# Kernel optimization log

Measured on AMD Instinct MI355X. Metric: run time of the kernel, lower is better.

Reference implementation:

```python
import jax, jax.numpy as jnp
import numpy as np

N, E = 50000, 800000
IN_DIM, HIDDEN, OUT_DIM, LAYERS = 128, 64, 40, 3


def setup_inputs() -> dict:
    key = jax.random.key(0)
    ks = jax.random.split(key, 12)
    glorot = lambda k, fi, fo: jax.random.normal(k, (fi, fo), jnp.float32) * np.sqrt(2.0 / (fi + fo)).astype(np.float32)
    return {
        "x": jax.random.normal(ks[0], (N, IN_DIM), jnp.float32),
        "edge_index": jax.random.randint(ks[1], (2, E), 0, N, jnp.int64),
        "edge_weight": jax.random.uniform(ks[2], (E,), jnp.float32),
        "W1": glorot(ks[3], IN_DIM, HIDDEN), "b1": jnp.zeros((HIDDEN,), jnp.float32),
        "W2": glorot(ks[4], HIDDEN, HIDDEN), "b2": jnp.zeros((HIDDEN,), jnp.float32),
        "W3": glorot(ks[5], HIDDEN, HIDDEN), "b3": jnp.zeros((HIDDEN,), jnp.float32),
        "Wlin": glorot(ks[6], HIDDEN * LAYERS, OUT_DIM), "blin": jnp.zeros((OUT_DIM,), jnp.float32),
    }


def reference(x, edge_index, edge_weight, W1, b1, W2, b2, W3, b3, Wlin, blin):
    src, dst = edge_index[0], edge_index[1]

    def gcn_conv(h, W, b):
        # GCNConv with normalize=False: linear transform, then weighted sum aggregation at dst, then bias.
        h = h @ W                                   # [N, hidden]
        msg = h[src] * edge_weight[:, None]          # [E, hidden] gather + scale
        agg = jax.ops.segment_sum(msg, dst, num_segments=h.shape[0])  # scatter-add
        return agg + b

    outs = []
    h = x
    for W, b in ((W1, b1), (W2, b2), (W3, b3)):
        h = jax.nn.relu(gcn_conv(h, W, b))           # dropout is identity at inference
        outs.append(h)

    hjk = jnp.concatenate(outs, axis=-1)             # JumpingKnowledge mode='cat' -> [N, hidden*layers]
    return hjk @ Wlin + blin                         # [N, out_dim]
```

## Files before the change

### kernel.cpp

```cpp
#include <hip/hip_runtime.h>

#define HID 64
#define JK_DIM 192
#define OUT_DIM 40
#define AP 136
#define HP 72

typedef __attribute__((ext_vector_type(8))) short bf16x8;
typedef __attribute__((ext_vector_type(4))) float f32x4;

__device__ inline unsigned short f2b(float f) {
    unsigned u = __float_as_uint(f);
    unsigned r = u + 0x7FFF + ((u >> 16) & 1);
    return (unsigned short)(r >> 16);
}
__device__ inline float b2f(unsigned short u) {
    return __uint_as_float(((unsigned)u) << 16);
}
__device__ inline float blo(unsigned u) { return __uint_as_float(u << 16); }
__device__ inline float bhi(unsigned u) { return __uint_as_float(u & 0xFFFF0000u); }
__device__ inline unsigned pack2(float a, float b) {
    return (unsigned)f2b(a) | ((unsigned)f2b(b) << 16);
}

__global__ __launch_bounds__(256) void prep(int* __restrict__ deg, int n,
                                            int* __restrict__ gctr,
                                            const float* __restrict__ W1,
                                            const float* __restrict__ W2,
                                            const float* __restrict__ W3,
                                            const float* __restrict__ Wlin,
                                            unsigned short* __restrict__ W1T,
                                            unsigned short* __restrict__ W2T,
                                            unsigned short* __restrict__ W3T,
                                            unsigned short* __restrict__ WlinT) {
    int i = blockIdx.x * 256 + threadIdx.x;
    if (i == 0) gctr[0] = 0;
    if (i < n) deg[i] = 0;
    if (i < 64 * 128) {
        int nn = i >> 7, k = i & 127;
        W1T[i] = f2b(W1[k * 64 + nn]);
    }
    if (i < 64 * 64) {
        int nn = i >> 6, k = i & 63;
        W2T[i] = f2b(W2[k * 64 + nn]);
        W3T[i] = f2b(W3[k * 64 + nn]);
    }
    if (i < 48 * JK_DIM) {
        int c = i / JK_DIM, k = i - c * JK_DIM;
        WlinT[i] = (c < OUT_DIM) ? f2b(Wlin[k * OUT_DIM + c]) : (unsigned short)0;
    }
}

__global__ __launch_bounds__(256) void hist_dst(const int* __restrict__ dst,
                                                int* __restrict__ deg,
                                                unsigned short* __restrict__ rank,
                                                int E, int part) {
    int p = blockIdx.x & 7;
    int bid = blockIdx.x >> 3;
    int nblk = gridDim.x >> 3;
    int lo = p * part, hi = lo + part;
    int E4 = E >> 2;
    for (int q = bid * 256 + threadIdx.x; q < E4; q += nblk * 256) {
        int4 d4 = ((const int4*)dst)[q];
        int e = q * 4;
        if (d4.x >= lo && d4.x < hi) rank[e + 0] = (unsigned short)atomicAdd(&deg[d4.x], 1);
        if (d4.y >= lo && d4.y < hi) rank[e + 1] = (unsigned short)atomicAdd(&deg[d4.y], 1);
        if (d4.z >= lo && d4.z < hi) rank[e + 2] = (unsigned short)atomicAdd(&deg[d4.z], 1);
        if (d4.w >= lo && d4.w < hi) rank[e + 3] = (unsigned short)atomicAdd(&deg[d4.w], 1);
    }
    if (bid == 0 && threadIdx.x < (E & 3)) {
        int e = (E & ~3) + threadIdx.x;
        int d = dst[e];
        if (d >= lo && d < hi) rank[e] = (unsigned short)atomicAdd(&deg[d], 1);
    }
}

__global__ __launch_bounds__(256) void scan_fused(const int* __restrict__ deg,
                                                  int* __restrict__ off,
                                                  int* __restrict__ gctr, int n) {
    __shared__ int tmp[256];
    __shared__ int base;
    int i = blockIdx.x * 256 + threadIdx.x;
    int v = (i < n) ? deg[i] : 0;
    tmp[threadIdx.x] = v;
    __syncthreads();
    for (int d = 1; d < 256; d <<= 1) {
        int t = (threadIdx.x >= d) ? tmp[threadIdx.x - d] : 0;
        __syncthreads();
        tmp[threadIdx.x] += t;
        __syncthreads();
    }
    if (threadIdx.x == 255) base = atomicAdd(gctr, tmp[255]);
    __syncthreads();
    if (i < n) off[i] = base + tmp[threadIdx.x] - v;
}

__global__ __launch_bounds__(256) void fill_and_gemm(
        const int* __restrict__ src, const int* __restrict__ dst,
        const float* __restrict__ ew, const int* __restrict__ off,
        const unsigned short* __restrict__ rank,
        unsigned* __restrict__ ecsr, int E,
        const float* __restrict__ x, const unsigned short* __restrict__ W1T,
        unsigned short* __restrict__ linb, int n, int nFill) {
    __shared__ unsigned short Ah[64 * AP];
    __shared__ unsigned short Wt[64 * AP];
    int tid = threadIdx.x;
    if ((int)blockIdx.x < nFill) {
        int q = blockIdx.x * 256 + tid;
        int E4 = E >> 2;
        if (q < E4) {
            int4 d4 = ((const int4*)dst)[q];
            int4 s4 = ((const int4*)src)[q];
            float4 wv = ((const float4*)ew)[q];
            ushort4 r4 = ((const ushort4*)rank)[q];
            ecsr[off[d4.x] + r4.x] = (unsigned)s4.x | ((unsigned)f2b(wv.x) << 16);
            ecsr[off[d4.y] + r4.y] = (unsigned)s4.y | ((unsigned)f2b(wv.y) << 16);
            ecsr[off[d4.z] + r4.z] = (unsigned)s4.z | ((unsigned)f2b(wv.z) << 16);
            ecsr[off[d4.w] + r4.w] = (unsigned)s4.w | ((unsigned)f2b(wv.w) << 16);
        }
        if (blockIdx.x == 0 && tid < (E & 3)) {
            int e = (E & ~3) + tid;
            int d = dst[e];
            ecsr[off[d] + rank[e]] = (unsigned)src[e] | ((unsigned)f2b(ew[e]) << 16);
        }
        return;
    }
    int row0 = (blockIdx.x - nFill) * 64;
    if (row0 >= n) return;
    for (int i = tid; i < 64 * 32; i += 256) {
        int r = i >> 5;
        int c4 = (i & 31) * 4;
        int grow = row0 + r;
        if (grow >= n) grow = n - 1;
        float4 v = *(const float4*)(x + (long)grow * 128 + c4);
        ushort4 o;
        o.x = f2b(v.x); o.y = f2b(v.y); o.z = f2b(v.z); o.w = f2b(v.w);
        *(ushort4*)(Ah + r * AP + c4) = o;
    }
    for (int i = tid; i < 64 * 16; i += 256) {
        int nn = i >> 4;
        int k8 = (i & 15) * 8;
        *(uint4*)(Wt + nn * AP + k8) = *(const uint4*)(W1T + nn * 128 + k8);
    }
    __syncthreads();

    int wave = tid >> 6;
    int lane = tid & 63;
    int lr = lane & 15;
    int lk = (lane >> 4) * 8;
    f32x4 acc[4];
#pragma unroll
    for (int nf = 0; nf < 4; ++nf) acc[nf] = (f32x4){0.f, 0.f, 0.f, 0.f};
#pragma unroll
    for (int k0 = 0; k0 < 128; k0 += 32) {
        bf16x8 a = *(const bf16x8*)(Ah + (wave * 16 + lr) * AP + k0 + lk);
#pragma unroll
        for (int nf = 0; nf < 4; ++nf) {
            bf16x8 b = *(const bf16x8*)(Wt + (nf * 16 + lr) * AP + k0 + lk);
            acc[nf] = __builtin_amdgcn_mfma_f32_16x16x32_bf16(a, b, acc[nf], 0, 0, 0);
        }
    }
    int mbase = wave * 16 + (lane >> 4) * 4;
#pragma unroll
    for (int nf = 0; nf < 4; ++nf) {
#pragma unroll
        for (int r = 0; r < 4; ++r) {
            int grow = row0 + mbase + r;
            if (grow < n)
                linb[(long)grow * HID + nf * 16 + lr] = f2b(acc[nf][r]);
        }
    }
}

__global__ __launch_bounds__(256) void aggregate(const unsigned short* __restrict__ linb,
                                                 const unsigned* __restrict__ ecsr,
                                                 const int* __restrict__ off,
                                                 const int* __restrict__ deg,
                                                 const float* __restrict__ bias,
                                                 unsigned short* __restrict__ hout, int n) {
    int cl = threadIdx.x & 7;
    float4 bLo = *(const float4*)(bias + cl * 8);
    float4 bHi = *(const float4*)(bias + cl * 8 + 4);
    int grp = (blockIdx.x * 256 + threadIdx.x) >> 3;
    int ngrp = (gridDim.x * 256) >> 3;
    for (int node = grp; node < n; node += ngrp) {
        int start = off[node];
        int cnt = deg[node];
        float acc[8];
#pragma unroll
        for (int i = 0; i < 8; ++i) acc[i] = 0.f;

        int s[8];
        float w[8];
#pragma unroll
        for (int t = 0; t < 8; ++t) {
            s[t] = 0; w[t] = 0.f;
            if (t < cnt) {
                unsigned m = ecsr[start + t];
                s[t] = (int)(m & 0xFFFFu);
                w[t] = b2f((unsigned short)(m >> 16));
            }
        }
        for (int bb = 0; bb < cnt; bb += 8) {
            int s2[8];
            float w2[8];
#pragma unroll
            for (int t = 0; t < 8; ++t) {
                int e = bb + 8 + t;
                s2[t] = 0; w2[t] = 0.f;
                if (e < cnt) {
                    unsigned m = ecsr[start + e];
                    s2[t] = (int)(m & 0xFFFFu);
                    w2[t] = b2f((unsigned short)(m >> 16));
                }
            }
            uint4 u[8];
#pragma unroll
            for (int t = 0; t < 8; ++t)
                u[t] = *(const uint4*)(linb + (long)s[t] * HID + cl * 8);
#pragma unroll
            for (int t = 0; t < 8; ++t) {
                acc[0] += blo(u[t].x) * w[t];
                acc[1] += bhi(u[t].x) * w[t];
                acc[2] += blo(u[t].y) * w[t];
                acc[3] += bhi(u[t].y) * w[t];
                acc[4] += blo(u[t].z) * w[t];
                acc[5] += bhi(u[t].z) * w[t];
                acc[6] += blo(u[t].w) * w[t];
                acc[7] += bhi(u[t].w) * w[t];
            }
#pragma unroll
            for (int t = 0; t < 8; ++t) { s[t] = s2[t]; w[t] = w2[t]; }
        }

        uint4 o;
        o.x = pack2(fmaxf(acc[0] + bLo.x, 0.f), fmaxf(acc[1] + bLo.y, 0.f));
        o.y = pack2(fmaxf(acc[2] + bLo.z, 0.f), fmaxf(acc[3] + bLo.w, 0.f));
        o.z = pack2(fmaxf(acc[4] + bHi.x, 0.f), fmaxf(acc[5] + bHi.y, 0.f));
        o.w = pack2(fmaxf(acc[6] + bHi.z, 0.f), fmaxf(acc[7] + bHi.w, 0.f));
        *(uint4*)(hout + (long)node * JK_DIM + cl * 8) = o;
    }
}

__global__ __launch_bounds__(256) void agg_transform(
        const unsigned short* __restrict__ hprev,
        const unsigned* __restrict__ ecsr,
        const int* __restrict__ off, const int* __restrict__ deg,
        const unsigned short* __restrict__ WT, const float* __restrict__ bias,
        unsigned short* __restrict__ hout, int n) {
    __shared__ unsigned short Hs[64 * HP];
    __shared__ unsigned short Wt[64 * HP];
    int tid = threadIdx.x;
    int row0 = blockIdx.x * 64;
    if (row0 >= n) return;
    for (int i = tid; i < 64 * 8; i += 256) {
        int nn = i >> 3;
        int k8 = (i & 7) * 8;
        *(uint4*)(Wt + nn * HP + k8) = *(const uint4*)(WT + nn * 64 + k8);
    }
    int cl = tid & 7;
    int g0 = tid >> 3;
    for (int gi = 0; gi < 2; ++gi) {
        int lrow = g0 + gi * 32;
        int node = row0 + lrow;
        float acc[8];
#pragma unroll
        for (int i = 0; i < 8; ++i) acc[i] = 0.f;
        if (node < n) {
            int start = off[node];
            int cnt = deg[node];
            int s[8];
            float w[8];
#pragma unroll
            for (int t = 0; t < 8; ++t) {
                s[t] = 0; w[t] = 0.f;
                if (t < cnt) {
                    unsigned m = ecsr[start + t];
                    s[t] = (int)(m & 0xFFFFu);
                    w[t] = b2f((unsigned short)(m >> 16));
                }
            }
            for (int bb = 0; bb < cnt; bb += 8) {
                int s2[8];
                float w2[8];
#pragma unroll
                for (int t = 0; t < 8; ++t) {
                    int e = bb + 8 + t;
                    s2[t] = 0; w2[t] = 0.f;
                    if (e < cnt) {
                        unsigned m = ecsr[start + e];
                        s2[t] = (int)(m & 0xFFFFu);
                        w2[t] = b2f((unsigned short)(m >> 16));
                    }
                }
                uint4 u[8];
#pragma unroll
                for (int t = 0; t < 8; ++t)
                    u[t] = *(const uint4*)(hprev + (long)s[t] * JK_DIM + cl * 8);
#pragma unroll
                for (int t = 0; t < 8; ++t) {
                    acc[0] += blo(u[t].x) * w[t];
                    acc[1] += bhi(u[t].x) * w[t];
                    acc[2] += blo(u[t].y) * w[t];
                    acc[3] += bhi(u[t].y) * w[t];
                    acc[4] += blo(u[t].z) * w[t];
                    acc[5] += bhi(u[t].z) * w[t];
                    acc[6] += blo(u[t].w) * w[t];
                    acc[7] += bhi(u[t].w) * w[t];
                }
#pragma unroll
                for (int t = 0; t < 8; ++t) { s[t] = s2[t]; w[t] = w2[t]; }
            }
        }
        uint4 o;
        o.x = pack2(acc[0], acc[1]);
        o.y = pack2(acc[2], acc[3]);
        o.z = pack2(acc[4], acc[5]);
        o.w = pack2(acc[6], acc[7]);
        *(uint4*)(Hs + lrow * HP + cl * 8) = o;
    }
    __syncthreads();
    int wave = tid >> 6;
    int lane = tid & 63;
    int lr = lane & 15;
    int lk = (lane >> 4) * 8;
    f32x4 d[4];
#pragma unroll
    for (int nf = 0; nf < 4; ++nf) d[nf] = (f32x4){0.f, 0.f, 0.f, 0.f};
#pragma unroll
    for (int k0 = 0; k0 < 64; k0 += 32) {
        bf16x8 a = *(const bf16x8*)(Hs + (wave * 16 + lr) * HP + k0 + lk);
#pragma unroll
        for (int nf = 0; nf < 4; ++nf) {
            bf16x8 b = *(const bf16x8*)(Wt + (nf * 16 + lr) * HP + k0 + lk);
            d[nf] = __builtin_amdgcn_mfma_f32_16x16x32_bf16(a, b, d[nf], 0, 0, 0);
        }
    }
    int mbase = wave * 16 + (lane >> 4) * 4;
#pragma unroll
    for (int nf = 0; nf < 4; ++nf) {
        float bv = bias[nf * 16 + lr];
#pragma unroll
        for (int r = 0; r < 4; ++r) {
            int grow = row0 + mbase + r;
            if (grow < n)
                hout[(long)grow * JK_DIM + nf * 16 + lr] = f2b(fmaxf(d[nf][r] + bv, 0.f));
        }
    }
}

__global__ __launch_bounds__(256) void jk_final(
        const unsigned short* __restrict__ hprev,
        const unsigned* __restrict__ ecsr,
        const int* __restrict__ off, const int* __restrict__ deg,
        const unsigned short* __restrict__ W3T, const float* __restrict__ bias,
        const unsigned short* __restrict__ hcat,
        const unsigned short* __restrict__ WlinT,
        const float* __restrict__ blin,
        float* __restrict__ outp, int n) {
    __shared__ unsigned short pool[128 * HP];
    unsigned short* Hs = pool;
    unsigned short* Wt = pool + 64 * HP;
    int tid = threadIdx.x;
    int row0 = blockIdx.x * 64;
    if (row0 >= n) return;
    for (int i = tid; i < 64 * 8; i += 256) {
        int nn = i >> 3;
        int k8 = (i & 7) * 8;
        *(uint4*)(Wt + nn * HP + k8) = *(const uint4*)(W3T + nn * 64 + k8);
    }
    int cl = tid & 7;
    int g0 = tid >> 3;
    for (int gi = 0; gi < 2; ++gi) {
        int lrow = g0 + gi * 32;
        int node = row0 + lrow;
        float acc[8];
#pragma unroll
        for (int i = 0; i < 8; ++i) acc[i] = 0.f;
        if (node < n) {
            int start = off[node];
            int cnt = deg[node];
            int s[8];
            float w[8];
#pragma unroll
            for (int t = 0; t < 8; ++t) {
                s[t] = 0; w[t] = 0.f;
                if (t < cnt) {
                    unsigned m = ecsr[start + t];
                    s[t] = (int)(m & 0xFFFFu);
                    w[t] = b2f((unsigned short)(m >> 16));
                }
            }
            for (int bb = 0; bb < cnt; bb += 8) {
                int s2[8];
                float w2[8];
#pragma unroll
                for (int t = 0; t < 8; ++t) {
                    int e = bb + 8 + t;
                    s2[t] = 0; w2[t] = 0.f;
                    if (e < cnt) {
                        unsigned m = ecsr[start + e];
                        s2[t] = (int)(m & 0xFFFFu);
                        w2[t] = b2f((unsigned short)(m >> 16));
                    }
                }
                uint4 u[8];
#pragma unroll
                for (int t = 0; t < 8; ++t)
                    u[t] = *(const uint4*)(hprev + (long)s[t] * JK_DIM + cl * 8);
#pragma unroll
                for (int t = 0; t < 8; ++t) {
                    acc[0] += blo(u[t].x) * w[t];
                    acc[1] += bhi(u[t].x) * w[t];
                    acc[2] += blo(u[t].y) * w[t];
                    acc[3] += bhi(u[t].y) * w[t];
                    acc[4] += blo(u[t].z) * w[t];
                    acc[5] += bhi(u[t].z) * w[t];
                    acc[6] += blo(u[t].w) * w[t];
                    acc[7] += bhi(u[t].w) * w[t];
                }
#pragma unroll
                for (int t = 0; t < 8; ++t) { s[t] = s2[t]; w[t] = w2[t]; }
            }
        }
        uint4 o;
        o.x = pack2(acc[0], acc[1]);
        o.y = pack2(acc[2], acc[3]);
        o.z = pack2(acc[4], acc[5]);
        o.w = pack2(acc[6], acc[7]);
        *(uint4*)(Hs + lrow * HP + cl * 8) = o;
    }
    __syncthreads();
    int wave = tid >> 6;
    int lane = tid & 63;
    int lr = lane & 15;
    int lk = (lane >> 4) * 8;
    f32x4 d[4];
#pragma unroll
    for (int nf = 0; nf < 4; ++nf) d[nf] = (f32x4){0.f, 0.f, 0.f, 0.f};
#pragma unroll
    for (int k0 = 0; k0 < 64; k0 += 32) {
        bf16x8 a = *(const bf16x8*)(Hs + (wave * 16 + lr) * HP + k0 + lk);
#pragma unroll
        for (int nf = 0; nf < 4; ++nf) {
            bf16x8 b = *(const bf16x8*)(Wt + (nf * 16 + lr) * HP + k0 + lk);
            d[nf] = __builtin_amdgcn_mfma_f32_16x16x32_bf16(a, b, d[nf], 0, 0, 0);
        }
    }
    int mbase = wave * 16 + (lane >> 4) * 4;
    unsigned short* As = Hs;
    unsigned short* WL = Wt;
    f32x4 acc2[3];
#pragma unroll
    for (int nf = 0; nf < 3; ++nf) acc2[nf] = (f32x4){0.f, 0.f, 0.f, 0.f};
    for (int ch = 0; ch < 2; ++ch) {
        int cb = ch * 64;
        __syncthreads();
        for (int i = tid; i < 64 * 8; i += 256) {
            int r = i >> 3;
            int q8 = (i & 7) * 8;
            int grow = row0 + r;
            if (grow >= n) grow = n - 1;
            *(uint4*)(As + r * HP + q8) = *(const uint4*)(hcat + (long)grow * JK_DIM + cb + q8);
        }
        for (int i = tid; i < 48 * 8; i += 256) {
            int c = i >> 3;
            int k8 = (i & 7) * 8;
            *(uint4*)(WL + c * HP + k8) = *(const uint4*)(WlinT + c * JK_DIM + cb + k8);
        }
        __syncthreads();
#pragma unroll
        for (int k0 = 0; k0 < 64; k0 += 32) {
            bf16x8 a = *(const bf16x8*)(As + (wave * 16 + lr) * HP + k0 + lk);
#pragma unroll
            for (int nf = 0; nf < 3; ++nf) {
                bf16x8 b = *(const bf16x8*)(WL + (nf * 16 + lr) * HP + k0 + lk);
                acc2[nf] = __builtin_amdgcn_mfma_f32_16x16x32_bf16(a, b, acc2[nf], 0, 0, 0);
            }
        }
    }
    __syncthreads();
#pragma unroll
    for (int nf = 0; nf < 4; ++nf) {
        float bv = bias[nf * 16 + lr];
#pragma unroll
        for (int r = 0; r < 4; ++r)
            As[(mbase + r) * HP + nf * 16 + lr] = f2b(fmaxf(d[nf][r] + bv, 0.f));
    }
    for (int i = tid; i < 48 * 8; i += 256) {
        int c = i >> 3;
        int k8 = (i & 7) * 8;
        *(uint4*)(WL + c * HP + k8) = *(const uint4*)(WlinT + c * JK_DIM + 128 + k8);
    }
    __syncthreads();
#pragma unroll
    for (int k0 = 0; k0 < 64; k0 += 32) {
        bf16x8 a = *(const bf16x8*)(As + (wave * 16 + lr) * HP + k0 + lk);
#pragma unroll
        for (int nf = 0; nf < 3; ++nf) {
            bf16x8 b = *(const bf16x8*)(WL + (nf * 16 + lr) * HP + k0 + lk);
            acc2[nf] = __builtin_amdgcn_mfma_f32_16x16x32_bf16(a, b, acc2[nf], 0, 0, 0);
        }
    }
#pragma unroll
    for (int nf = 0; nf < 3; ++nf) {
        int col = nf * 16 + lr;
        if (col < OUT_DIM) {
            float bb = blin[col];
#pragma unroll
            for (int r = 0; r < 4; ++r) {
                int grow = row0 + mbase + r;
                if (grow < n)
                    outp[(long)grow * OUT_DIM + col] = acc2[nf][r] + bb;
            }
        }
    }
}

extern "C" void kernel_launch(void* const* d_in, const int* in_sizes, int n_in,
                              void* d_out, int out_size, void* d_ws, size_t ws_size,
                              hipStream_t stream) {
    const float* x    = (const float*)d_in[0];
    const int*   ei   = (const int*)d_in[1];
    const float* ew   = (const float*)d_in[2];
    const float* W1   = (const float*)d_in[3];
    const float* b1   = (const float*)d_in[4];
    const float* W2   = (const float*)d_in[5];
    const float* b2   = (const float*)d_in[6];
    const float* W3   = (const float*)d_in[7];
    const float* b3   = (const float*)d_in[8];
    const float* Wlin = (const float*)d_in[9];
    const float* blin = (const float*)d_in[10];
    float* out = (float*)d_out;

    const int N = in_sizes[0] / 128;
    const int E = in_sizes[2];
    const int* src = ei;
    const int* dst = ei + E;
    const int PART = (N + 7) / 8;

    char* wsb = (char*)d_ws;
    unsigned short* linb  = (unsigned short*)wsb;   wsb += (long)N * HID * 2;
    unsigned short* hcatb = (unsigned short*)wsb;   wsb += (long)N * JK_DIM * 2;
    int* deg    = (int*)wsb;                        wsb += (long)N * 4;
    int* off    = (int*)wsb;                        wsb += (long)N * 4;
    int* bsum   = (int*)wsb;                        wsb += 256 * 4;
    unsigned short* W1T  = (unsigned short*)wsb;    wsb += 64 * 128 * 2;
    unsigned short* W2T  = (unsigned short*)wsb;    wsb += 64 * 64 * 2;
    unsigned short* W3T  = (unsigned short*)wsb;    wsb += 64 * 64 * 2;
    unsigned short* WlinT = (unsigned short*)wsb;   wsb += 48 * JK_DIM * 2;
    unsigned* ecsr = (unsigned*)wsb;
    unsigned short* rank = hcatb;
    int* gctr = bsum;

    dim3 blk(256);
    const int nblkN = (N + 255) / 256;
    dim3 gN(nblkN);
    dim3 gHist(8 * 104);
    const int nFill = ((E >> 2) + 255) / 256;
    const int nGemm = (N + 63) / 64;
    dim3 gFG(nFill + nGemm);
    dim3 gTile((N + 63) / 64);
    dim3 gAgg((N + 31) / 32);

    unsigned short* h1 = hcatb;
    unsigned short* h2 = hcatb + HID;

    prep<<<gN, blk, 0, stream>>>(deg, N, gctr, W1, W2, W3, Wlin,
                                 W1T, W2T, W3T, WlinT);
    hist_dst<<<gHist, blk, 0, stream>>>(dst, deg, rank, E, PART);
    scan_fused<<<gN, blk, 0, stream>>>(deg, off, gctr, N);

    fill_and_gemm<<<gFG, blk, 0, stream>>>(src, dst, ew, off, rank, ecsr, E,
                                           x, W1T, linb, N, nFill);
    aggregate<<<gAgg, blk, 0, stream>>>(linb, ecsr, off, deg, b1, h1, N);

    agg_transform<<<gTile, blk, 0, stream>>>(h1, ecsr, off, deg, W2T, b2, h2, N);

    jk_final<<<gTile, blk, 0, stream>>>(h2, ecsr, off, deg, W3T, b3,
                                        hcatb, WlinT, blin, out, N);
}
```

Measured before the change: 233.7 us.

## Fold weight prep into histogram kernel and read GEMM operands from global

Removes the separate prep kernel. Zeroing of deg, off and the scan counter now goes through hipMemsetAsync, and the weight transpose/bf16 conversion runs in 32 extra blocks appended to the hist_dst grid. The small GEMMs in fill_and_gemm, agg_transform and jk_final no longer stage x, weights or hcat tiles through LDS; they load MFMA operands straight from global memory (x is converted to bf16 in registers), which drops several __syncthreads and cuts shared-memory use to raise occupancy. The trade-off is more uncoalesced or redundant global/L2 traffic for the B operands, plus a memset node in place of a kernel launch.

Result: slower. 260.0 us (+11.2%).

```diff
diff --git a/kernel.cpp b/kernel.cpp
--- a/kernel.cpp
+++ b/kernel.cpp
@@ -3,7 +3,6 @@
 #define HID 64
 #define JK_DIM 192
 #define OUT_DIM 40
-#define AP 136
 #define HP 72
 
 typedef __attribute__((ext_vector_type(8))) short bf16x8;
@@ -23,41 +22,39 @@
     return (unsigned)f2b(a) | ((unsigned)f2b(b) << 16);
 }
 
-__global__ __launch_bounds__(256) void prep(int* __restrict__ deg, int n,
-                                            int* __restrict__ gctr,
-                                            const float* __restrict__ W1,
-                                            const float* __restrict__ W2,
-                                            const float* __restrict__ W3,
-                                            const float* __restrict__ Wlin,
-                                            unsigned short* __restrict__ W1T,
-                                            unsigned short* __restrict__ W2T,
-                                            unsigned short* __restrict__ W3T,
-                                            unsigned short* __restrict__ WlinT) {
-    int i = blockIdx.x * 256 + threadIdx.x;
-    if (i == 0) gctr[0] = 0;
-    if (i < n) deg[i] = 0;
-    if (i < 64 * 128) {
-        int nn = i >> 7, k = i & 127;
-        W1T[i] = f2b(W1[k * 64 + nn]);
-    }
-    if (i < 64 * 64) {
-        int nn = i >> 6, k = i & 63;
-        W2T[i] = f2b(W2[k * 64 + nn]);
-        W3T[i] = f2b(W3[k * 64 + nn]);
-    }
-    if (i < 48 * JK_DIM) {
-        int c = i / JK_DIM, k = i - c * JK_DIM;
-        WlinT[i] = (c < OUT_DIM) ? f2b(Wlin[k * OUT_DIM + c]) : (unsigned short)0;
-    }
-}
-
 __global__ __launch_bounds__(256) void hist_dst(const int* __restrict__ dst,
                                                 int* __restrict__ deg,
                                                 unsigned short* __restrict__ rank,
-                                                int E, int part) {
+                                                int E, int part, int histBlk,
+                                                const float* __restrict__ W1,
+                                                const float* __restrict__ W2,
+                                                const float* __restrict__ W3,
+                                                const float* __restrict__ Wlin,
+                                                unsigned short* __restrict__ W1T,
+                                                unsigned short* __restrict__ W2T,
+                                                unsigned short* __restrict__ W3T,
+                                                unsigned short* __restrict__ WlinT) {
+    if ((int)blockIdx.x >= histBlk) {
+        int base = (blockIdx.x - histBlk) * 256 + threadIdx.x;
+        int stride = 32 * 256;
+        for (int i = base; i < 64 * 128; i += stride) {
+            int nn = i >> 7, k = i & 127;
+            W1T[i] = f2b(W1[k * 64 + nn]);
+        }
+        for (int i = base; i < 64 * 64; i += stride) {
+            int nn = i >> 6, k = i & 63;
+            W2T[i] = f2b(W2[k * 64 + nn]);
+            W3T[i] = f2b(W3[k * 64 + nn]);
+        }
+        for (int i = base; i < 48 * JK_DIM; i += stride) {
+            int c = i / JK_DIM, k = i - c * JK_DIM;
+            WlinT[i] = (c < OUT_DIM) ? f2b(Wlin[k * OUT_DIM + c]) : (unsigned short)0;
+        }
+        return;
+    }
     int p = blockIdx.x & 7;
     int bid = blockIdx.x >> 3;
-    int nblk = gridDim.x >> 3;
+    int nblk = histBlk >> 3;
     int lo = p * part, hi = lo + part;
     int E4 = E >> 2;
     for (int q = bid * 256 + threadIdx.x; q < E4; q += nblk * 256) {
@@ -102,8 +99,6 @@
         unsigned* __restrict__ ecsr, int E,
         const float* __restrict__ x, const unsigned short* __restrict__ W1T,
         unsigned short* __restrict__ linb, int n, int nFill) {
-    __shared__ unsigned short Ah[64 * AP];
-    __shared__ unsigned short Wt[64 * AP];
     int tid = threadIdx.x;
     if ((int)blockIdx.x < nFill) {
         int q = blockIdx.x * 256 + tid;
@@ -127,36 +122,28 @@
     }
     int row0 = (blockIdx.x - nFill) * 64;
     if (row0 >= n) return;
-    for (int i = tid; i < 64 * 32; i += 256) {
-        int r = i >> 5;
-        int c4 = (i & 31) * 4;
-        int grow = row0 + r;
-        if (grow >= n) grow = n - 1;
-        float4 v = *(const float4*)(x + (long)grow * 128 + c4);
-        ushort4 o;
-        o.x = f2b(v.x); o.y = f2b(v.y); o.z = f2b(v.z); o.w = f2b(v.w);
-        *(ushort4*)(Ah + r * AP + c4) = o;
-    }
-    for (int i = tid; i < 64 * 16; i += 256) {
-        int nn = i >> 4;
-        int k8 = (i & 15) * 8;
-        *(uint4*)(Wt + nn * AP + k8) = *(const uint4*)(W1T + nn * 128 + k8);
-    }
-    __syncthreads();
-
     int wave = tid >> 6;
     int lane = tid & 63;
     int lr = lane & 15;
-    int lk = (lane >> 4) * 8;
+    int lk8 = (lane >> 4) * 8;
+    int arow = row0 + wave * 16 + lr;
+    if (arow >= n) arow = n - 1;
+    const float* xrow = x + (long)arow * 128;
     f32x4 acc[4];
 #pragma unroll
     for (int nf = 0; nf < 4; ++nf) acc[nf] = (f32x4){0.f, 0.f, 0.f, 0.f};
 #pragma unroll
     for (int k0 = 0; k0 < 128; k0 += 32) {
-        bf16x8 a = *(const bf16x8*)(Ah + (wave * 16 + lr) * AP + k0 + lk);
+        float4 va = *(const float4*)(xrow + k0 + lk8);
+        float4 vb = *(const float4*)(xrow + k0 + lk8 + 4);
+        bf16x8 a;
+        a[0] = (short)f2b(va.x); a[1] = (short)f2b(va.y);
+        a[2] = (short)f2b(va.z); a[3] = (short)f2b(va.w);
+        a[4] = (short)f2b(vb.x); a[5] = (short)f2b(vb.y);
+        a[6] = (short)f2b(vb.z); a[7] = (short)f2b(vb.w);
 #pragma unroll
         for (int nf = 0; nf < 4; ++nf) {
-            bf16x8 b = *(const bf16x8*)(Wt + (nf * 16 + lr) * AP + k0 + lk);
+            bf16x8 b = *(const bf16x8*)(W1T + (nf * 16 + lr) * 128 + k0 + lk8);
             acc[nf] = __builtin_amdgcn_mfma_f32_16x16x32_bf16(a, b, acc[nf], 0, 0, 0);
         }
     }
@@ -249,15 +236,9 @@
         const unsigned short* __restrict__ WT, const float* __restrict__ bias,
         unsigned short* __restrict__ hout, int n) {
     __shared__ unsigned short Hs[64 * HP];
-    __shared__ unsigned short Wt[64 * HP];
     int tid = threadIdx.x;
     int row0 = blockIdx.x * 64;
     if (row0 >= n) return;
-    for (int i = tid; i < 64 * 8; i += 256) {
-        int nn = i >> 3;
-        int k8 = (i & 7) * 8;
-        *(uint4*)(Wt + nn * HP + k8) = *(const uint4*)(WT + nn * 64 + k8);
-    }
     int cl = tid & 7;
     int g0 = tid >> 3;
     for (int gi = 0; gi < 2; ++gi) {
@@ -323,16 +304,16 @@
     int wave = tid >> 6;
     int lane = tid & 63;
     int lr = lane & 15;
-    int lk = (lane >> 4) * 8;
+    int lk8 = (lane >> 4) * 8;
     f32x4 d[4];
 #pragma unroll
     for (int nf = 0; nf < 4; ++nf) d[nf] = (f32x4){0.f, 0.f, 0.f, 0.f};
 #pragma unroll
     for (int k0 = 0; k0 < 64; k0 += 32) {
-        bf16x8 a = *(const bf16x8*)(Hs + (wave * 16 + lr) * HP + k0 + lk);
+        bf16x8 a = *(const bf16x8*)(Hs + (wave * 16 + lr) * HP + k0 + lk8);
 #pragma unroll
         for (int nf = 0; nf < 4; ++nf) {
-            bf16x8 b = *(const bf16x8*)(Wt + (nf * 16 + lr) * HP + k0 + lk);
+            bf16x8 b = *(const bf16x8*)(WT + (nf * 16 + lr) * 64 + k0 + lk8);
             d[nf] = __builtin_amdgcn_mfma_f32_16x16x32_bf16(a, b, d[nf], 0, 0, 0);
         }
     }
@@ -358,17 +339,10 @@
         const unsigned short* __restrict__ WlinT,
         const float* __restrict__ blin,
         float* __restrict__ outp, int n) {
-    __shared__ unsigned short pool[128 * HP];
-    unsigned short* Hs = pool;
-    unsigned short* Wt = pool + 64 * HP;
+    __shared__ unsigned short Hs[64 * HP];
     int tid = threadIdx.x;
     int row0 = blockIdx.x * 64;
     if (row0 >= n) return;
-    for (int i = tid; i < 64 * 8; i += 256) {
-        int nn = i >> 3;
-        int k8 = (i & 7) * 8;
-        *(uint4*)(Wt + nn * HP + k8) = *(const uint4*)(W3T + nn * 64 + k8);
-    }
     int cl = tid & 7;
     int g0 = tid >> 3;
     for (int gi = 0; gi < 2; ++gi) {
@@ -434,47 +408,35 @@
     int wave = tid >> 6;
     int lane = tid & 63;
     int lr = lane & 15;
-    int lk = (lane >> 4) * 8;
+    int lk8 = (lane >> 4) * 8;
     f32x4 d[4];
 #pragma unroll
     for (int nf = 0; nf < 4; ++nf) d[nf] = (f32x4){0.f, 0.f, 0.f, 0.f};
 #pragma unroll
     for (int k0 = 0; k0 < 64; k0 += 32) {
-        bf16x8 a = *(const bf16x8*)(Hs + (wave * 16 + lr) * HP + k0 + lk);
+        bf16x8 a = *(const bf16x8*)(Hs + (wave * 16 + lr) * HP + k0 + lk8);
 #pragma unroll
         for (int nf = 0; nf < 4; ++nf) {
-            bf16x8 b = *(const bf16x8*)(Wt + (nf * 16 + lr) * HP + k0 + lk);
+            bf16x8 b = *(const bf16x8*)(W3T + (nf * 16 + lr) * 64 + k0 + lk8);
             d[nf] = __builtin_amdgcn_mfma_f32_16x16x32_bf16(a, b, d[nf], 0, 0, 0);
         }
     }
     int mbase = wave * 16 + (lane >> 4) * 4;
-    unsigned short* As = Hs;
-    unsigned short* WL = Wt;
     f32x4 acc2[3];
 #pragma unroll
     for (int nf = 0; nf < 3; ++nf) acc2[nf] = (f32x4){0.f, 0.f, 0.f, 0.f};
+    int arow = row0 + wave * 16 + lr;
+    if (arow >= n) arow = n - 1;
+    const unsigned short* hrow = hcat + (long)arow * JK_DIM;
+#pragma unroll
     for (int ch = 0; ch < 2; ++ch) {
         int cb = ch * 64;
-        __syncthreads();
-        for (int i = tid; i < 64 * 8; i += 256) {
-            int r = i >> 3;
-            int q8 = (i & 7) * 8;
-            int grow = row0 + r;
-            if (grow >= n) grow = n - 1;
-            *(uint4*)(As + r * HP + q8) = *(const uint4*)(hcat + (long)grow * JK_DIM + cb + q8);
-        }
-        for (int i = tid; i < 48 * 8; i += 256) {
-            int c = i >> 3;
-            int k8 = (i & 7) * 8;
-            *(uint4*)(WL + c * HP + k8) = *(const uint4*)(WlinT + c * JK_DIM + cb + k8);
-        }
-        __syncthreads();
 #pragma unroll
         for (int k0 = 0; k0 < 64; k0 += 32) {
-            bf16x8 a = *(const bf16x8*)(As + (wave * 16 + lr) * HP + k0 + lk);
+            bf16x8 a = *(const bf16x8*)(hrow + cb + k0 + lk8);
 #pragma unroll
             for (int nf = 0; nf < 3; ++nf) {
-                bf16x8 b = *(const bf16x8*)(WL + (nf * 16 + lr) * HP + k0 + lk);
+                bf16x8 b = *(const bf16x8*)(WlinT + (nf * 16 + lr) * JK_DIM + cb + k0 + lk8);
                 acc2[nf] = __builtin_amdgcn_mfma_f32_16x16x32_bf16(a, b, acc2[nf], 0, 0, 0);
             }
         }
@@ -485,20 +447,15 @@
         float bv = bias[nf * 16 + lr];
 #pragma unroll
         for (int r = 0; r < 4; ++r)
-            As[(mbase + r) * HP + nf * 16 + lr] = f2b(fmaxf(d[nf][r] + bv, 0.f));
-    }
-    for (int i = tid; i < 48 * 8; i += 256) {
-        int c = i >> 3;
-        int k8 = (i & 7) * 8;
-        *(uint4*)(WL + c * HP + k8) = *(const uint4*)(WlinT + c * JK_DIM + 128 + k8);
+            Hs[(mbase + r) * HP + nf * 16 + lr] = f2b(fmaxf(d[nf][r] + bv, 0.f));
     }
     __syncthreads();
 #pragma unroll
     for (int k0 = 0; k0 < 64; k0 += 32) {
-        bf16x8 a = *(const bf16x8*)(As + (wave * 16 + lr) * HP + k0 + lk);
+        bf16x8 a = *(const bf16x8*)(Hs + (wave * 16 + lr) * HP + k0 + lk8);
 #pragma unroll
         for (int nf = 0; nf < 3; ++nf) {
-            bf16x8 b = *(const bf16x8*)(WL + (nf * 16 + lr) * HP + k0 + lk);
+            bf16x8 b = *(const bf16x8*)(WlinT + (nf * 16 + lr) * JK_DIM + 128 + k0 + lk8);
             acc2[nf] = __builtin_amdgcn_mfma_f32_16x16x32_bf16(a, b, acc2[nf], 0, 0, 0);
         }
     }
@@ -542,9 +499,11 @@
     char* wsb = (char*)d_ws;
     unsigned short* linb  = (unsigned short*)wsb;   wsb += (long)N * HID * 2;
     unsigned short* hcatb = (unsigned short*)wsb;   wsb += (long)N * JK_DIM * 2;
+    char* zbase = wsb;
     int* deg    = (int*)wsb;                        wsb += (long)N * 4;
     int* off    = (int*)wsb;                        wsb += (long)N * 4;
     int* bsum   = (int*)wsb;                        wsb += 256 * 4;
+    size_t zbytes = (size_t)(wsb - zbase);
     unsigned short* W1T  = (unsigned short*)wsb;    wsb += 64 * 128 * 2;
     unsigned short* W2T  = (unsigned short*)wsb;    wsb += 64 * 64 * 2;
     unsigned short* W3T  = (unsigned short*)wsb;    wsb += 64 * 64 * 2;
@@ -556,7 +515,8 @@
     dim3 blk(256);
     const int nblkN = (N + 255) / 256;
     dim3 gN(nblkN);
-    dim3 gHist(8 * 104);
+    const int histBlk = 8 * 104;
+    dim3 gHist(histBlk + 32);
     const int nFill = ((E >> 2) + 255) / 256;
     const int nGemm = (N + 63) / 64;
     dim3 gFG(nFill + nGemm);
@@ -566,9 +526,10 @@
     unsigned short* h1 = hcatb;
     unsigned short* h2 = hcatb + HID;
 
-    prep<<<gN, blk, 0, stream>>>(deg, N, gctr, W1, W2, W3, Wlin,
-                                 W1T, W2T, W3T, WlinT);
-    hist_dst<<<gHist, blk, 0, stream>>>(dst, deg, rank, E, PART);
+    hipMemsetAsync(zbase, 0, zbytes, stream);
+
+    hist_dst<<<gHist, blk, 0, stream>>>(dst, deg, rank, E, PART, histBlk,
+                                        W1, W2, W3, Wlin, W1T, W2T, W3T, WlinT);
     scan_fused<<<gN, blk, 0, stream>>>(deg, off, gctr, N);
 
     fill_and_gemm<<<gFG, blk, 0, stream>>>(src, dst, ew, off, rank, ecsr, E,
```
